# Kernel optimization log

Hardware: AMD Instinct MI355X
Metric: run time of the kernel (lower is better)

## Reference

```python
import jax, jax.numpy as jnp
import numpy as np

N_NODES = 100000
N_EDGES = 1600000
IN = 128
HID = 128
EPS = 1e-5


def setup_inputs() -> dict:
    key = jax.random.key(0)
    ks = jax.random.split(key, 20)
    def lin(k, fi, fo):
        return jax.random.normal(k, (fi, fo), dtype=jnp.float32) / np.sqrt(fi)
    inp = {
        'x': jax.random.normal(ks[0], (N_NODES, IN), dtype=jnp.float32),
        'src': jax.random.randint(ks[1], (N_EDGES,), 0, N_NODES),
        'dst': jax.random.randint(ks[2], (N_EDGES,), 0, N_NODES),
        # SAGEConv layer 1..3: fc_self, fc_neigh, bias
        'Wself1': lin(ks[3], IN, HID), 'Wneigh1': lin(ks[4], IN, HID), 'b1': jnp.zeros((HID,), jnp.float32),
        'Wself2': lin(ks[5], HID, HID), 'Wneigh2': lin(ks[6], HID, HID), 'b2': jnp.zeros((HID,), jnp.float32),
        'Wself3': lin(ks[7], HID, HID), 'Wneigh3': lin(ks[8], HID, HID), 'b3': jnp.zeros((HID,), jnp.float32),
        # shared BatchNorm1d(hid)
        'gamma': jnp.ones((HID,), jnp.float32), 'beta': jnp.zeros((HID,), jnp.float32),
        # decoder MLP hid->hid->hid->1
        'Wd1': lin(ks[9], HID, HID), 'bd1': jnp.zeros((HID,), jnp.float32),
        'Wd2': lin(ks[10], HID, HID), 'bd2': jnp.zeros((HID,), jnp.float32),
        'Wd3': lin(ks[11], HID, 1), 'bd3': jnp.zeros((1,), jnp.float32),
    }
    return inp


def _sage_conv(h, src, dst, deg, Wself, Wneigh, b, n):
    # mean aggregation over in-neighbors: gather + segment-sum + divide
    neigh_sum = jax.ops.segment_sum(h[src], dst, num_segments=n)  # [N, F]
    neigh_mean = neigh_sum / deg[:, None]
    return h @ Wself + neigh_mean @ Wneigh + b


def _batch_norm(h, gamma, beta):
    mu = jnp.mean(h, axis=0)
    var = jnp.mean(jnp.square(h - mu), axis=0)  # biased var, as torch BN training
    return gamma * (h - mu) * jax.lax.rsqrt(var + EPS) + beta


def reference(x, src, dst, Wself1, Wneigh1, b1, Wself2, Wneigh2, b2,
              Wself3, Wneigh3, b3, gamma, beta, Wd1, bd1, Wd2, bd2, Wd3, bd3):
    n = x.shape[0]
    deg = jax.ops.segment_sum(jnp.ones_like(dst, dtype=x.dtype), dst, num_segments=n)
    deg = jnp.maximum(deg, 1.0)
    h = _sage_conv(x, src, dst, deg, Wself1, Wneigh1, b1, n)
    h = jax.nn.relu(_batch_norm(h, gamma, beta))  # dropout = identity (eval)
    h = _sage_conv(h, src, dst, deg, Wself2, Wneigh2, b2, n)
    h = jax.nn.relu(_batch_norm(h, gamma, beta))
    h = _sage_conv(h, src, dst, deg, Wself3, Wneigh3, b3, n)
    # decoder MLP
    h = jax.nn.relu(h @ Wd1 + bd1)
    h = jax.nn.relu(h @ Wd2 + bd2)
    return h @ Wd3 + bd3  # [N, 1]
```

## Files before the change

### kernel.cpp

```cpp
#include <hip/hip_runtime.h>

typedef unsigned short u16;
typedef unsigned int u32;
using bf16x8 = __attribute__((ext_vector_type(8))) __bf16;
using f32x4  = __attribute__((ext_vector_type(4))) float;
using u32x4  = __attribute__((ext_vector_type(4))) u32;
using u32x2  = __attribute__((ext_vector_type(2))) u32;

#define CAP 48
#define LDSROW 136

__global__ void SAGE_79328045957727_kernel() {}

__device__ __forceinline__ float bf2f(u16 u) {
  union { u32 i; float f; } v; v.i = ((u32)u) << 16; return v.f;
}
__device__ __forceinline__ u16 f2bf(float f) {
  union { float f; u32 i; } v; v.f = f;
  u32 x = v.i;
  return (u16)((x + 0x7FFFu + ((x >> 16) & 1u)) >> 16);
}


__global__ void zero_kernel(int* p, int n) {
  int i = blockIdx.x * 256 + threadIdx.x;
  if (i < n) p[i] = 0;
}


__global__ __launch_bounds__(256) void build_kernel(
    const int* __restrict__ src, const int* __restrict__ dst,
    int* __restrict__ deg, int* __restrict__ csr, int E, int npart,
    const float* __restrict__ x, u16* __restrict__ xb, long nelem4,
    const float* w0, const float* w1, const float* w2, const float* w3,
    const float* w4, const float* w5, const float* w6, const float* w7,
    u16* __restrict__ wt) {
  int b = blockIdx.x;
  if (b < 1024) {
    int p = b & 7;
    int brank = b >> 3;
    int lo = p * npart, hi = lo + npart;
    int E4 = E >> 2;
    for (int i = brank * 256 + threadIdx.x; i < E4; i += 128 * 256) {
      u32x4 d4 = __builtin_nontemporal_load((const u32x4*)dst + i);
      u32x4 s4 = __builtin_nontemporal_load((const u32x4*)src + i);
#pragma unroll
      for (int k = 0; k < 4; ++k) {
        int dv = (int)d4[k];
        if (dv >= lo && dv < hi) {
          int pos = atomicAdd(&deg[dv], 1);
          if (pos < CAP) csr[(size_t)dv * CAP + pos] = (int)s4[k];
        }
      }
    }
    for (int i = (E4 << 2) + brank * 256 + threadIdx.x; i < E; i += 128 * 256) {
      int dv = dst[i];
      if (dv >= lo && dv < hi) {
        int pos = atomicAdd(&deg[dv], 1);
        if (pos < CAP) csr[(size_t)dv * CAP + pos] = src[i];
      }
    }
  } else if (b < 1280) {
    long t = (long)(b - 1024) * 256 + threadIdx.x;
    for (long i4 = t; i4 < nelem4; i4 += 256 * 256) {
      f32x4 v = __builtin_nontemporal_load((const f32x4*)x + i4);
      u32x2 o;
      o[0] = ((u32)f2bf(v[1]) << 16) | (u32)f2bf(v[0]);
      o[1] = ((u32)f2bf(v[3]) << 16) | (u32)f2bf(v[2]);
      __builtin_nontemporal_store(o, (u32x2*)(xb + i4 * 4));
    }
  } else {
    int tg = (b - 1280) * 256 + threadIdx.x;
    for (int k = 0; k < 8; ++k) {
      int idx = tg + k * 16384;
      int m = idx >> 14;
      int i = idx & 16383;
      const float* W = m == 0 ? w0 : m == 1 ? w1 : m == 2 ? w2 : m == 3 ? w3
                     : m == 4 ? w4 : m == 5 ? w5 : m == 6 ? w6 : w7;
      int r = i >> 7, c = i & 127;
      wt[(size_t)m * 16384 + (size_t)c * 128 + r] = f2bf(W[i]);
    }
  }
}


__global__ __launch_bounds__(256) void bnrelu_kernel(
    const u16* __restrict__ Z, u16* __restrict__ G,
    const float* __restrict__ stats, const float* __restrict__ gamma,
    const float* __restrict__ beta, long n4, float invN) {
  __shared__ float sSc[128], sSh[128];
  int t = threadIdx.x;
  if (t < 128) {
    float mu = stats[t] * invN;
    float var = stats[128 + t] * invN - mu * mu;
    float is = rsqrtf(var + 1e-5f);
    float sc = gamma[t] * is;
    sSc[t] = sc;
    sSh[t] = beta[t] - mu * sc;
  }
  __syncthreads();
  for (long i4 = (long)blockIdx.x * 256 + t; i4 < n4; i4 += (long)gridDim.x * 256) {
    uint4 q = ((const uint4*)Z)[i4];
    int c0 = ((int)(i4 & 15)) * 8;
    float e0 = fmaxf(sSc[c0+0]*bf2f((u16)(q.x & 0xffffu))+sSh[c0+0], 0.f);
    float e1 = fmaxf(sSc[c0+1]*bf2f((u16)(q.x >> 16))    +sSh[c0+1], 0.f);
    float e2 = fmaxf(sSc[c0+2]*bf2f((u16)(q.y & 0xffffu))+sSh[c0+2], 0.f);
    float e3 = fmaxf(sSc[c0+3]*bf2f((u16)(q.y >> 16))    +sSh[c0+3], 0.f);
    float e4 = fmaxf(sSc[c0+4]*bf2f((u16)(q.z & 0xffffu))+sSh[c0+4], 0.f);
    float e5 = fmaxf(sSc[c0+5]*bf2f((u16)(q.z >> 16))    +sSh[c0+5], 0.f);
    float e6 = fmaxf(sSc[c0+6]*bf2f((u16)(q.w & 0xffffu))+sSh[c0+6], 0.f);
    float e7 = fmaxf(sSc[c0+7]*bf2f((u16)(q.w >> 16))    +sSh[c0+7], 0.f);
    uint4 o;
    o.x = ((u32)f2bf(e1) << 16) | (u32)f2bf(e0);
    o.y = ((u32)f2bf(e3) << 16) | (u32)f2bf(e2);
    o.z = ((u32)f2bf(e5) << 16) | (u32)f2bf(e4);
    o.w = ((u32)f2bf(e7) << 16) | (u32)f2bf(e6);
    ((uint4*)G)[i4] = o;
  }
}


__global__ __launch_bounds__(256) void gather_kernel(
    const u16* __restrict__ G, const int* __restrict__ csr,
    const int* __restrict__ deg, u16* __restrict__ M, int N) {
  int node = blockIdx.x * 16 + (threadIdx.x >> 4);
  if (node >= N) return;
  int lane = threadIdx.x & 15;
  int fo = lane * 8;
  const int* nl = csr + (size_t)node * CAP;
  int d = deg[node];
  int dm = d < CAP ? d : CAP;
  float a0=0.f,a1=0.f,a2=0.f,a3=0.f,a4=0.f,a5=0.f,a6=0.f,a7=0.f;

#define ACC8(q) do { \
    a0 += bf2f((u16)((q).x & 0xffffu)); a1 += bf2f((u16)((q).x >> 16)); \
    a2 += bf2f((u16)((q).y & 0xffffu)); a3 += bf2f((u16)((q).y >> 16)); \
    a4 += bf2f((u16)((q).z & 0xffffu)); a5 += bf2f((u16)((q).z >> 16)); \
    a6 += bf2f((u16)((q).w & 0xffffu)); a7 += bf2f((u16)((q).w >> 16)); \
  } while (0)

  int e = 0;
  for (; e + 8 <= dm; e += 8) {
    int ia = nl[e+0], ib = nl[e+1], ic = nl[e+2], id_ = nl[e+3];
    int ie_ = nl[e+4], if_ = nl[e+5], ig = nl[e+6], ih = nl[e+7];
    uint4 q0 = *(const uint4*)(G + (size_t)ia  * 128 + fo);
    uint4 q1 = *(const uint4*)(G + (size_t)ib  * 128 + fo);
    uint4 q2 = *(const uint4*)(G + (size_t)ic  * 128 + fo);
    uint4 q3 = *(const uint4*)(G + (size_t)id_ * 128 + fo);
    uint4 q4 = *(const uint4*)(G + (size_t)ie_ * 128 + fo);
    uint4 q5 = *(const uint4*)(G + (size_t)if_ * 128 + fo);
    uint4 q6 = *(const uint4*)(G + (size_t)ig  * 128 + fo);
    uint4 q7 = *(const uint4*)(G + (size_t)ih  * 128 + fo);
    ACC8(q0); ACC8(q1); ACC8(q2); ACC8(q3);
    ACC8(q4); ACC8(q5); ACC8(q6); ACC8(q7);
  }
  if (e + 4 <= dm) {
    int ia = nl[e+0], ib = nl[e+1], ic = nl[e+2], id_ = nl[e+3];
    uint4 q0 = *(const uint4*)(G + (size_t)ia  * 128 + fo);
    uint4 q1 = *(const uint4*)(G + (size_t)ib  * 128 + fo);
    uint4 q2 = *(const uint4*)(G + (size_t)ic  * 128 + fo);
    uint4 q3 = *(const uint4*)(G + (size_t)id_ * 128 + fo);
    ACC8(q0); ACC8(q1); ACC8(q2); ACC8(q3);
    e += 4;
  }
  for (; e < dm; ++e) {
    uint4 q = *(const uint4*)(G + (size_t)nl[e] * 128 + fo);
    ACC8(q);
  }
#undef ACC8

  float inv = 1.f / (float)(d > 0 ? d : 1);
  uint4 o;
  o.x = ((u32)f2bf(a1 * inv) << 16) | (u32)f2bf(a0 * inv);
  o.y = ((u32)f2bf(a3 * inv) << 16) | (u32)f2bf(a2 * inv);
  o.z = ((u32)f2bf(a5 * inv) << 16) | (u32)f2bf(a4 * inv);
  o.w = ((u32)f2bf(a7 * inv) << 16) | (u32)f2bf(a6 * inv);
  *(uint4*)(M + (size_t)node * 128 + fo) = o;
}


__device__ __forceinline__ void stage_tile(
    const u16* __restrict__ A, u16* sT, size_t row0, int N, int tid) {
  for (int j = 0; j < 8; ++j) {
    int idx = j * 1024 + tid * 4;
    int r = idx >> 6;
    int c = idx & 63;
    size_t grow = row0 + r;
    if (grow >= (size_t)N) grow = (size_t)(N - 1);
    const u32* gp = (const u32*)(A + grow * 128) + c;
    u32 v0 = gp[0], v1 = gp[1], v2 = gp[2], v3 = gp[3];
    u32* lp = (u32*)(sT + (size_t)r * LDSROW + c * 2);
    lp[0] = v0; lp[1] = v1; lp[2] = v2; lp[3] = v3;
  }
}

__device__ __forceinline__ void preload_tile(
    const u16* __restrict__ A, u32 rb[8][4], size_t row0, int N, int tid) {
  for (int j = 0; j < 8; ++j) {
    int idx = j * 1024 + tid * 4;
    int r = idx >> 6;
    int c = idx & 63;
    size_t grow = row0 + r;
    if (grow >= (size_t)N) grow = (size_t)(N - 1);
    const u32* gp = (const u32*)(A + grow * 128) + c;
    rb[j][0] = gp[0]; rb[j][1] = gp[1]; rb[j][2] = gp[2]; rb[j][3] = gp[3];
  }
}

__device__ __forceinline__ void write_tile(
    const u32 rb[8][4], u16* sT, int tid) {
  for (int j = 0; j < 8; ++j) {
    int idx = j * 1024 + tid * 4;
    int r = idx >> 6;
    int c = idx & 63;
    u32* lp = (u32*)(sT + (size_t)r * LDSROW + c * 2);
    lp[0] = rb[j][0]; lp[1] = rb[j][1]; lp[2] = rb[j][2]; lp[3] = rb[j][3];
  }
}

__device__ __forceinline__ void mfma_tile(
    const u16* sT, const u16* __restrict__ Wt, f32x4 acc[8][2],
    int wave, int l15, int quad) {
  bf16x8 wf[2][4];
  for (int ct = 0; ct < 2; ++ct) {
    int col = wave * 32 + ct * 16 + l15;
    for (int kk = 0; kk < 4; ++kk)
      wf[ct][kk] = *(const bf16x8*)(Wt + (size_t)col * 128 + kk * 32 + quad * 8);
  }
  for (int kk = 0; kk < 4; ++kk) {
    int kbase = kk * 32 + quad * 8;
    for (int rt = 0; rt < 8; ++rt) {
      bf16x8 af = *(const bf16x8*)(sT + (size_t)(rt * 16 + l15) * LDSROW + kbase);
      acc[rt][0] = __builtin_amdgcn_mfma_f32_16x16x32_bf16(af, wf[0][kk], acc[rt][0], 0, 0, 0);
      acc[rt][1] = __builtin_amdgcn_mfma_f32_16x16x32_bf16(af, wf[1][kk], acc[rt][1], 0, 0, 0);
    }
  }
}


__global__ __launch_bounds__(256) void gemm2(
    const u16* __restrict__ A, const u16* __restrict__ B,
    const u16* __restrict__ W1t, const u16* __restrict__ W2t,
    const float* __restrict__ bias, u16* __restrict__ C,
    float* __restrict__ statsOut, int N) {
  __shared__ u16 sT[128 * LDSROW];
  int tid = threadIdx.x;
  int wave = tid >> 6;
  int lane = tid & 63;
  int l15 = lane & 15;
  int quad = lane >> 4;
  size_t row0 = (size_t)blockIdx.x * 128;

  f32x4 acc[8][2];
  for (int rt = 0; rt < 8; ++rt)
    for (int ct = 0; ct < 2; ++ct)
      for (int i = 0; i < 4; ++i) acc[rt][ct][i] = 0.f;

  u32 rb[8][4];
  preload_tile(B, rb, row0, N, tid);
  stage_tile(A, sT, row0, N, tid);
  __syncthreads();
  mfma_tile(sT, W1t, acc, wave, l15, quad);
  __syncthreads();
  write_tile(rb, sT, tid);
  __syncthreads();
  mfma_tile(sT, W2t, acc, wave, l15, quad);

  for (int ct = 0; ct < 2; ++ct) {
    int col = wave * 32 + ct * 16 + l15;
    float bv = bias[col];
    float ssum = 0.f, ssq = 0.f;
    for (int rt = 0; rt < 8; ++rt) {
      for (int i = 0; i < 4; ++i) {
        size_t row = row0 + rt * 16 + quad * 4 + i;
        if (row < (size_t)N) {
          float v = acc[rt][ct][i] + bv;
          C[row * 128 + col] = f2bf(v);
          ssum += v; ssq += v * v;
        }
      }
    }
    for (int o = 16; o < 64; o <<= 1) {
      ssum += __shfl_xor(ssum, o);
      ssq  += __shfl_xor(ssq, o);
    }
    if (quad == 0) {
      atomicAdd(&statsOut[col], ssum);
      atomicAdd(&statsOut[128 + col], ssq);
    }
  }
}


__global__ __launch_bounds__(256) void megagemm(
    const u16* __restrict__ G, const u16* __restrict__ M,
    const u16* __restrict__ wtS3, const u16* __restrict__ wtN3,
    const float* __restrict__ b3,
    const u16* __restrict__ wtD1, const float* __restrict__ bd1,
    const u16* __restrict__ wtD2, const float* __restrict__ bd2,
    const float* __restrict__ wd3, const float* __restrict__ bd3,
    float* __restrict__ outF, int N) {
  __shared__ u16 sT[128 * LDSROW];
  __shared__ float sOut[128];

  int tid = threadIdx.x;
  int wave = tid >> 6;
  int lane = tid & 63;
  int l15 = lane & 15;
  int quad = lane >> 4;
  size_t row0 = (size_t)blockIdx.x * 128;

  if (tid < 128) sOut[tid] = 0.f;

  f32x4 acc[8][2];
  for (int rt = 0; rt < 8; ++rt)
    for (int ct = 0; ct < 2; ++ct)
      for (int i = 0; i < 4; ++i) acc[rt][ct][i] = 0.f;

  u32 rb[8][4];
  preload_tile(G, rb, row0, N, tid);
  stage_tile(M, sT, row0, N, tid);
  __syncthreads();
  mfma_tile(sT, wtN3, acc, wave, l15, quad);
  __syncthreads();
  write_tile(rb, sT, tid);
  __syncthreads();
  mfma_tile(sT, wtS3, acc, wave, l15, quad);

  for (int g = 0; g < 2; ++g) {
    const u16* Wt = g ? wtD2 : wtD1;
    const float* bs = g ? bd1 : b3;
    int do_relu = g;

    __syncthreads();
    for (int ct = 0; ct < 2; ++ct) {
      int col = wave * 32 + ct * 16 + l15;
      float bv = bs[col];
      for (int rt = 0; rt < 8; ++rt) {
        for (int i = 0; i < 4; ++i) {
          int row = rt * 16 + quad * 4 + i;
          float v = acc[rt][ct][i] + bv;
          if (do_relu) v = fmaxf(v, 0.f);
          sT[(size_t)row * LDSROW + col] = f2bf(v);
        }
      }
    }
    __syncthreads();

    for (int rt = 0; rt < 8; ++rt)
      for (int ct = 0; ct < 2; ++ct)
        for (int i = 0; i < 4; ++i) acc[rt][ct][i] = 0.f;
    mfma_tile(sT, Wt, acc, wave, l15, quad);
  }

  {
    int col0 = wave * 32 + l15;
    float bv0 = bd2[col0], bv1 = bd2[col0 + 16];
    float w30 = wd3[col0], w31 = wd3[col0 + 16];
    for (int rt = 0; rt < 8; ++rt) {
      for (int i = 0; i < 4; ++i) {
        size_t row = row0 + rt * 16 + quad * 4 + i;
        float v0 = fmaxf(acc[rt][0][i] + bv0, 0.f);
        float v1 = fmaxf(acc[rt][1][i] + bv1, 0.f);
        float pv = v0 * w30 + v1 * w31;
        pv += __shfl_xor(pv, 1);
        pv += __shfl_xor(pv, 2);
        pv += __shfl_xor(pv, 4);
        pv += __shfl_xor(pv, 8);
        if (l15 == 0 && row < (size_t)N)
          atomicAdd(&sOut[rt * 16 + quad * 4 + i], pv);
      }
    }
    __syncthreads();
    if (tid < 128) {
      size_t row = row0 + tid;
      if (row < (size_t)N) outF[row] = sOut[tid] + bd3[0];
    }
  }
}


extern "C" void kernel_launch(void* const* d_in, const int* in_sizes, int n_in,
                              void* d_out, int out_size, void* d_ws, size_t ws_size,
                              hipStream_t stream) {
  const float* x      = (const float*)d_in[0];
  const int*   src    = (const int*)d_in[1];
  const int*   dst    = (const int*)d_in[2];
  const float* Wself1 = (const float*)d_in[3];
  const float* Wneigh1= (const float*)d_in[4];
  const float* b1     = (const float*)d_in[5];
  const float* Wself2 = (const float*)d_in[6];
  const float* Wneigh2= (const float*)d_in[7];
  const float* b2     = (const float*)d_in[8];
  const float* Wself3 = (const float*)d_in[9];
  const float* Wneigh3= (const float*)d_in[10];
  const float* b3     = (const float*)d_in[11];
  const float* gamma  = (const float*)d_in[12];
  const float* beta   = (const float*)d_in[13];
  const float* Wd1    = (const float*)d_in[14];
  const float* bd1    = (const float*)d_in[15];
  const float* Wd2    = (const float*)d_in[16];
  const float* bd2    = (const float*)d_in[17];
  const float* Wd3    = (const float*)d_in[18];
  const float* bd3    = (const float*)d_in[19];
  float* out = (float*)d_out;

  int N = in_sizes[0] / 128;
  int E = in_sizes[1];
  int npart = (N + 7) / 8;

  char* ws = (char*)d_ws;
  size_t off = 0;
  int* deg; int* csr; float* stats1; float* stats2;
  u16* xb; u16* ZA; u16* ZB; u16* M; u16* wt;
  deg   = (int*)(ws + off);   off += (size_t)N * 4;
  stats1= (float*)(ws + off); off += 256 * 4;
  stats2= (float*)(ws + off); off += 256 * 4;
  off = (off + 511) & ~(size_t)511;
  csr  = (int*)(ws + off);   off += ((size_t)N * CAP * 4 + 511) & ~(size_t)511;
  wt   = (u16*)(ws + off);   off += ((size_t)8 * 16384 * 2 + 511) & ~(size_t)511;
  xb   = (u16*)(ws + off);   off += ((size_t)N * 128 * 2 + 511) & ~(size_t)511;
  ZA   = (u16*)(ws + off);   off += ((size_t)N * 128 * 2 + 511) & ~(size_t)511;
  ZB   = (u16*)(ws + off);   off += ((size_t)N * 128 * 2 + 511) & ~(size_t)511;
  M    = (u16*)(ws + off);   off += ((size_t)N * 128 * 2 + 511) & ~(size_t)511;

  u16* wtS1 = wt + 0 * 16384; u16* wtN1 = wt + 1 * 16384;
  u16* wtS2 = wt + 2 * 16384; u16* wtN2 = wt + 3 * 16384;
  u16* wtS3 = wt + 4 * 16384; u16* wtN3 = wt + 5 * 16384;
  u16* wtD1 = wt + 6 * 16384; u16* wtD2 = wt + 7 * 16384;

  zero_kernel<<<(N + 512 + 255) / 256, 256, 0, stream>>>(deg, N + 512);

  long nelem4 = (long)N * 128 / 4;
  build_kernel<<<1344, 256, 0, stream>>>(
      src, dst, deg, csr, E, npart, x, xb, nelem4,
      Wself1, Wneigh1, Wself2, Wneigh2, Wself3, Wneigh3, Wd1, Wd2, wt);

  int strips = (N + 127) / 128;
  int g16    = (N + 15) / 16;
  float invN = 1.f / (float)N;
  long n4 = (long)N * 16;

  gather_kernel<<<g16, 256, 0, stream>>>(xb, csr, deg, M, N);
  gemm2<<<strips, 256, 0, stream>>>(xb, M, wtS1, wtN1, b1, ZA, stats1, N);

  bnrelu_kernel<<<2048, 256, 0, stream>>>(ZA, ZA, stats1, gamma, beta, n4, invN);

  gather_kernel<<<g16, 256, 0, stream>>>(ZA, csr, deg, M, N);
  gemm2<<<strips, 256, 0, stream>>>(ZA, M, wtS2, wtN2, b2, ZB, stats2, N);

  bnrelu_kernel<<<2048, 256, 0, stream>>>(ZB, ZB, stats2, gamma, beta, n4, invN);

  gather_kernel<<<g16, 256, 0, stream>>>(ZB, csr, deg, M, N);
  megagemm<<<strips, 256, 0, stream>>>(
      ZB, M, wtS3, wtN3, b3, wtD1, bd1, wtD2, bd2, Wd3, bd3, out, N);
}
```

Baseline: 523.7 us.

## Fuse BatchNorm+ReLU into GEMM via grid-wide barrier, keeping accumulators in registers

The separate bnrelu pass is removed. The GEMM kernel now accumulates column statistics, waits at a software grid barrier built on an atomic counter, computes the BN scale and shift, and writes the normalized, ReLU'd bf16 output straight from registers. This drops one full write and one read-modify-write of the N×128 activation per layer, plus a kernel launch. It relies on all 782 blocks being co-resident (launch_bounds(256,4) is meant to help), which risks deadlock if occupancy is not enough. The barrier wait can also idle compute units.

```diff
diff --git a/kernel.cpp b/kernel.cpp
--- a/kernel.cpp
+++ b/kernel.cpp
@@ -84,42 +84,6 @@
 }
 
 
-__global__ __launch_bounds__(256) void bnrelu_kernel(
-    const u16* __restrict__ Z, u16* __restrict__ G,
-    const float* __restrict__ stats, const float* __restrict__ gamma,
-    const float* __restrict__ beta, long n4, float invN) {
-  __shared__ float sSc[128], sSh[128];
-  int t = threadIdx.x;
-  if (t < 128) {
-    float mu = stats[t] * invN;
-    float var = stats[128 + t] * invN - mu * mu;
-    float is = rsqrtf(var + 1e-5f);
-    float sc = gamma[t] * is;
-    sSc[t] = sc;
-    sSh[t] = beta[t] - mu * sc;
-  }
-  __syncthreads();
-  for (long i4 = (long)blockIdx.x * 256 + t; i4 < n4; i4 += (long)gridDim.x * 256) {
-    uint4 q = ((const uint4*)Z)[i4];
-    int c0 = ((int)(i4 & 15)) * 8;
-    float e0 = fmaxf(sSc[c0+0]*bf2f((u16)(q.x & 0xffffu))+sSh[c0+0], 0.f);
-    float e1 = fmaxf(sSc[c0+1]*bf2f((u16)(q.x >> 16))    +sSh[c0+1], 0.f);
-    float e2 = fmaxf(sSc[c0+2]*bf2f((u16)(q.y & 0xffffu))+sSh[c0+2], 0.f);
-    float e3 = fmaxf(sSc[c0+3]*bf2f((u16)(q.y >> 16))    +sSh[c0+3], 0.f);
-    float e4 = fmaxf(sSc[c0+4]*bf2f((u16)(q.z & 0xffffu))+sSh[c0+4], 0.f);
-    float e5 = fmaxf(sSc[c0+5]*bf2f((u16)(q.z >> 16))    +sSh[c0+5], 0.f);
-    float e6 = fmaxf(sSc[c0+6]*bf2f((u16)(q.w & 0xffffu))+sSh[c0+6], 0.f);
-    float e7 = fmaxf(sSc[c0+7]*bf2f((u16)(q.w >> 16))    +sSh[c0+7], 0.f);
-    uint4 o;
-    o.x = ((u32)f2bf(e1) << 16) | (u32)f2bf(e0);
-    o.y = ((u32)f2bf(e3) << 16) | (u32)f2bf(e2);
-    o.z = ((u32)f2bf(e5) << 16) | (u32)f2bf(e4);
-    o.w = ((u32)f2bf(e7) << 16) | (u32)f2bf(e6);
-    ((uint4*)G)[i4] = o;
-  }
-}
-
-
 __global__ __launch_bounds__(256) void gather_kernel(
     const u16* __restrict__ G, const int* __restrict__ csr,
     const int* __restrict__ deg, u16* __restrict__ M, int N) {
@@ -238,12 +202,15 @@
 }
 
 
-__global__ __launch_bounds__(256) void gemm2(
+__global__ __launch_bounds__(256, 4) void gemmbn(
     const u16* __restrict__ A, const u16* __restrict__ B,
     const u16* __restrict__ W1t, const u16* __restrict__ W2t,
-    const float* __restrict__ bias, u16* __restrict__ C,
-    float* __restrict__ statsOut, int N) {
+    const float* __restrict__ bias, u16* __restrict__ G,
+    float* __restrict__ stats, int* __restrict__ bar,
+    const float* __restrict__ gamma, const float* __restrict__ beta,
+    int N, float invN, int nblk) {
   __shared__ u16 sT[128 * LDSROW];
+  __shared__ float sSc[128], sSh[128];
   int tid = threadIdx.x;
   int wave = tid >> 6;
   int lane = tid & 63;
@@ -275,7 +242,6 @@
         size_t row = row0 + rt * 16 + quad * 4 + i;
         if (row < (size_t)N) {
           float v = acc[rt][ct][i] + bv;
-          C[row * 128 + col] = f2bf(v);
           ssum += v; ssq += v * v;
         }
       }
@@ -285,8 +251,48 @@
       ssq  += __shfl_xor(ssq, o);
     }
     if (quad == 0) {
-      atomicAdd(&statsOut[col], ssum);
-      atomicAdd(&statsOut[128 + col], ssq);
+      atomicAdd(&stats[col], ssum);
+      atomicAdd(&stats[128 + col], ssq);
+    }
+  }
+
+  __threadfence();
+  __syncthreads();
+  if (tid == 0) {
+    __hip_atomic_fetch_add(bar, 1, __ATOMIC_ACQ_REL, __HIP_MEMORY_SCOPE_AGENT);
+    while (__hip_atomic_load(bar, __ATOMIC_ACQUIRE, __HIP_MEMORY_SCOPE_AGENT) < nblk)
+      __builtin_amdgcn_s_sleep(2);
+  }
+  __syncthreads();
+
+  if (tid < 128) {
+    union { u32 i; float f; } r1, r2;
+    r1.i = __hip_atomic_load((const u32*)&stats[tid], __ATOMIC_RELAXED,
+                             __HIP_MEMORY_SCOPE_AGENT);
+    r2.i = __hip_atomic_load((const u32*)&stats[128 + tid], __ATOMIC_RELAXED,
+                             __HIP_MEMORY_SCOPE_AGENT);
+    float mu = r1.f * invN;
+    float var = r2.f * invN - mu * mu;
+    float is = rsqrtf(var + 1e-5f);
+    float sc = gamma[tid] * is;
+    sSc[tid] = sc;
+    sSh[tid] = beta[tid] - mu * sc;
+  }
+  __syncthreads();
+
+  for (int ct = 0; ct < 2; ++ct) {
+    int col = wave * 32 + ct * 16 + l15;
+    float bv = bias[col];
+    float sc = sSc[col], sh = sSh[col];
+    for (int rt = 0; rt < 8; ++rt) {
+      for (int i = 0; i < 4; ++i) {
+        size_t row = row0 + rt * 16 + quad * 4 + i;
+        if (row < (size_t)N) {
+          float v = bf2f(f2bf(acc[rt][ct][i] + bv));
+          float g = fmaxf(sc * v + sh, 0.f);
+          G[row * 128 + col] = f2bf(g);
+        }
+      }
     }
   }
 }
@@ -411,11 +417,12 @@
 
   char* ws = (char*)d_ws;
   size_t off = 0;
-  int* deg; int* csr; float* stats1; float* stats2;
+  int* deg; int* csr; float* stats1; float* stats2; int* bars;
   u16* xb; u16* ZA; u16* ZB; u16* M; u16* wt;
   deg   = (int*)(ws + off);   off += (size_t)N * 4;
   stats1= (float*)(ws + off); off += 256 * 4;
   stats2= (float*)(ws + off); off += 256 * 4;
+  bars  = (int*)(ws + off);   off += 16 * 4;
   off = (off + 511) & ~(size_t)511;
   csr  = (int*)(ws + off);   off += ((size_t)N * CAP * 4 + 511) & ~(size_t)511;
   wt   = (u16*)(ws + off);   off += ((size_t)8 * 16384 * 2 + 511) & ~(size_t)511;
@@ -429,7 +436,7 @@
   u16* wtS3 = wt + 4 * 16384; u16* wtN3 = wt + 5 * 16384;
   u16* wtD1 = wt + 6 * 16384; u16* wtD2 = wt + 7 * 16384;
 
-  zero_kernel<<<(N + 512 + 255) / 256, 256, 0, stream>>>(deg, N + 512);
+  zero_kernel<<<(N + 512 + 16 + 255) / 256, 256, 0, stream>>>(deg, N + 512 + 16);
 
   long nelem4 = (long)N * 128 / 4;
   build_kernel<<<1344, 256, 0, stream>>>(
@@ -439,17 +446,14 @@
   int strips = (N + 127) / 128;
   int g16    = (N + 15) / 16;
   float invN = 1.f / (float)N;
-  long n4 = (long)N * 16;
 
   gather_kernel<<<g16, 256, 0, stream>>>(xb, csr, deg, M, N);
-  gemm2<<<strips, 256, 0, stream>>>(xb, M, wtS1, wtN1, b1, ZA, stats1, N);
-
-  bnrelu_kernel<<<2048, 256, 0, stream>>>(ZA, ZA, stats1, gamma, beta, n4, invN);
+  gemmbn<<<strips, 256, 0, stream>>>(
+      xb, M, wtS1, wtN1, b1, ZA, stats1, bars + 0, gamma, beta, N, invN, strips);
 
   gather_kernel<<<g16, 256, 0, stream>>>(ZA, csr, deg, M, N);
-  gemm2<<<strips, 256, 0, stream>>>(ZA, M, wtS2, wtN2, b2, ZB, stats2, N);
-
-  bnrelu_kernel<<<2048, 256, 0, stream>>>(ZB, ZB, stats2, gamma, beta, n4, invN);
+  gemmbn<<<strips, 256, 0, stream>>>(
+      ZA, M, wtS2, wtN2, b2, ZB, stats2, bars + 1, gamma, beta, N, invN, strips);
 
   gather_kernel<<<g16, 256, 0, stream>>>(ZB, csr, deg, M, N);
   megagemm<<<strips, 256, 0, stream>>>(
```

After: 797.1 us. 1.52x slower.
